# Kernel tuning notes

Measured on AMD Instinct MI355X. Metric: run time of the kernel, lower is better.

## Reference

```python
import jax, jax.numpy as jnp
import numpy as np

N_NODES = 65536
N_EDGES = 1048576
NODE_F = 32
EDGE_F = 8
HID = 64
OUT_F = 1
BATCH_SIZE = 64


def _glorot(key, shape):
    fan_in, fan_out = shape[0], shape[-1]
    s = jnp.sqrt(6.0 / (fan_in + fan_out))
    return jax.random.uniform(key, shape, jnp.float32, -s, s)


def setup_inputs() -> dict:
    key = jax.random.key(0)
    ks = jax.random.split(key, 20)
    inp = {
        "node_features": jax.random.normal(ks[0], (N_NODES, NODE_F), jnp.float32),
        "edge_features": jax.random.normal(ks[1], (N_EDGES, EDGE_F), jnp.float32),
        "Esrc": jax.random.randint(ks[2], (N_EDGES,), 0, N_NODES, jnp.int32),
        "Etgt": jax.random.randint(ks[3], (N_EDGES,), 0, N_NODES, jnp.int32),
        "batch": jnp.sort(jax.random.randint(ks[4], (N_NODES,), 0, BATCH_SIZE, jnp.int32)),
        # graph-conv weights
        "W_in": _glorot(ks[5], (NODE_F, HID)), "b_in": jnp.zeros((HID,), jnp.float32),
        "W_mid": _glorot(ks[6], (HID, HID)), "b_mid": jnp.zeros((HID,), jnp.float32),
        "W_out": _glorot(ks[7], (HID, OUT_F)), "b_out": jnp.zeros((OUT_F,), jnp.float32),
        # edge-encoder MLPs (Linear -> ReLU -> Linear)
        "ee_in_W1": _glorot(ks[8], (EDGE_F, HID)), "ee_in_b1": jnp.zeros((HID,), jnp.float32),
        "ee_in_W2": _glorot(ks[9], (HID, HID)), "ee_in_b2": jnp.zeros((HID,), jnp.float32),
        "ee_mid_W1": _glorot(ks[10], (EDGE_F, HID)), "ee_mid_b1": jnp.zeros((HID,), jnp.float32),
        "ee_mid_W2": _glorot(ks[11], (HID, HID)), "ee_mid_b2": jnp.zeros((HID,), jnp.float32),
        "ee_out_W1": _glorot(ks[12], (EDGE_F, OUT_F)), "ee_out_b1": jnp.zeros((OUT_F,), jnp.float32),
        "ee_out_W2": _glorot(ks[13], (OUT_F, OUT_F)), "ee_out_b2": jnp.zeros((OUT_F,), jnp.float32),
    }
    return inp


def _edge_mlp(ef, W1, b1, W2, b2):
    return jax.nn.relu(ef @ W1 + b1) @ W2 + b2  # [E, out]


def _egconv(x, W, b, Esrc, Etgt, edge_enc):
    support = x @ W                      # [N, out]
    msg = support[Esrc] * edge_enc       # [E, out] edge-gated messages
    agg = jax.ops.segment_sum(msg, Etgt, num_segments=N_NODES)  # [N, out]
    return agg + b


def reference(node_features, edge_features, Esrc, Etgt, batch,
              W_in, b_in, W_mid, b_mid, W_out, b_out,
              ee_in_W1, ee_in_b1, ee_in_W2, ee_in_b2,
              ee_mid_W1, ee_mid_b1, ee_mid_W2, ee_mid_b2,
              ee_out_W1, ee_out_b1, ee_out_W2, ee_out_b2):
    efin = _edge_mlp(edge_features, ee_in_W1, ee_in_b1, ee_in_W2, ee_in_b2)
    efmid = _edge_mlp(edge_features, ee_mid_W1, ee_mid_b1, ee_mid_W2, ee_mid_b2)
    efout = _edge_mlp(edge_features, ee_out_W1, ee_out_b1, ee_out_W2, ee_out_b2)

    x = jax.nn.relu(_egconv(node_features, W_in, b_in, Esrc, Etgt, efin))
    # dropout: identity in eval mode
    x = jax.nn.relu(_egconv(x, W_mid, b_mid, Esrc, Etgt, efmid))
    x = _egconv(x, W_out, b_out, Esrc, Etgt, efout)
    # graph-level sum pooling over batch ids
    out = jax.ops.segment_sum(x, batch, num_segments=BATCH_SIZE)  # [B, OUT_F]
    return out
```

## Files before the change

### kernel.cpp

```cpp
#include <hip/hip_runtime.h>

#define NN 65536
#define NE 1048576
#define NODE_F 32
#define EDGE_F 8
#define HID 64
#define NBATCH 64
#define NB 512
#define EPB (NE / NB)
#define NBIN 1024
#define CAP 2048

typedef __attribute__((ext_vector_type(8))) short s16x8;
typedef __attribute__((ext_vector_type(4))) float f32x4;

union FragU { s16x8 s; uint u[4]; };

__device__ inline uint pk2(float a, float b) {
    uint ua = __float_as_uint(a); ua += 0x7FFFu + ((ua >> 16) & 1u);
    uint ub = __float_as_uint(b); ub += 0x7FFFu + ((ub >> 16) & 1u);
    return (ua >> 16) | (ub & 0xFFFF0000u);
}

template<int K, bool RELUB>
__global__ __launch_bounds__(256) void node_linear(const float* __restrict__ x,
                                                   const float* __restrict__ pb,
                                                   const float* __restrict__ W,
                                                   float* __restrict__ out, int n_nodes) {
    const int lane = threadIdx.x & 63;
    const int wv = threadIdx.x >> 6;
    float wr[K];
#pragma unroll
    for (int k = 0; k < K; ++k) wr[k] = W[k * HID + lane];
    int wid = blockIdx.x * 4 + wv;
    const int nw = gridDim.x * 4;
    for (int n0 = wid; n0 < n_nodes; n0 += nw) {
        const int n = __builtin_amdgcn_readfirstlane(n0);
        const float* xr = x + (size_t)n * K;
        float acc = 0.f;
#pragma unroll
        for (int k = 0; k < K; ++k) {
            float xk = xr[k];
            if (RELUB) xk = fmaxf(xk + pb[k], 0.f);
            acc = fmaf(xk, wr[k], acc);
        }
        out[(size_t)n * HID + lane] = acc;
    }
}

__global__ __launch_bounds__(256) void p1_hist(const int* __restrict__ Etgt, int* __restrict__ bc,
                                               int* __restrict__ binTotal) {
    __shared__ int h[NBIN];
    const int blk = blockIdx.x;
    for (int t = threadIdx.x; t < NBIN; t += 256) h[t] = 0;
    __syncthreads();
    const int base = blk * EPB;
    for (int j = threadIdx.x; j < EPB; j += 256)
        atomicAdd(&h[((uint)Etgt[base + j]) >> 6], 1);
    __syncthreads();
    for (int t = threadIdx.x; t < NBIN; t += 256) {
        bc[blk * NBIN + t] = h[t];
        if (h[t]) atomicAdd(&binTotal[t], h[t]);
    }
}

__global__ __launch_bounds__(1024) void p2a_scan(const int* __restrict__ binTotal,
                                                 int* __restrict__ binStart) {
    __shared__ int part[NBIN];
    const int t = threadIdx.x;
    part[t] = binTotal[t];
    __syncthreads();
    for (int d = 1; d < NBIN; d <<= 1) {
        int v = part[t];
        int vo = (t >= d) ? part[t - d] : 0;
        __syncthreads();
        part[t] = v + vo;
        __syncthreads();
    }
    binStart[t + 1] = part[t];
    if (t == 0) binStart[0] = 0;
}

__global__ __launch_bounds__(256) void p2b_cursor(const int* __restrict__ bc,
                                                  const int* __restrict__ binStart,
                                                  int* __restrict__ cursor) {
    const int lane = threadIdx.x & 63;
    const int wv = threadIdx.x >> 6;
    const int bin = blockIdx.x * 4 + wv;
    int carry = binStart[bin];
    for (int c = 0; c < NB; c += 64) {
        const int blk = c + lane;
        const int v = bc[blk * NBIN + bin];
        int incl = v;
#pragma unroll
        for (int d = 1; d < 64; d <<= 1) {
            const int u = __shfl_up(incl, d, 64);
            if (lane >= d) incl += u;
        }
        cursor[blk * NBIN + bin] = carry + incl - v;
        carry += __shfl(incl, 63, 64);
    }
}

__global__ __launch_bounds__(256) void p3_scatter(
    const int* __restrict__ Etgt, const int* __restrict__ Esrc, const float* __restrict__ ef,
    const int* __restrict__ cursor, uint4* __restrict__ ef16_t, uint* __restrict__ stp_t)
{
    __shared__ int cur[NBIN];
    const int blk = blockIdx.x;
    for (int t = threadIdx.x; t < NBIN; t += 256) cur[t] = cursor[blk * NBIN + t];
    __syncthreads();
    const int base = blk * EPB;
    for (int j = threadIdx.x; j < EPB; j += 256) {
        const int i = base + j;
        const int tgt = Etgt[i];
        const int p = atomicAdd(&cur[(uint)tgt >> 6], 1);
        const float4 x = *(const float4*)(ef + (size_t)i * 8);
        const float4 y = *(const float4*)(ef + (size_t)i * 8 + 4);
        uint4 u;
        u.x = pk2(x.x, x.y); u.y = pk2(x.z, x.w);
        u.z = pk2(y.x, y.y); u.w = pk2(y.z, y.w);
        ef16_t[p] = u;
        stp_t[p] = (uint)Esrc[i] | ((uint)tgt << 16);
    }
}

__global__ __launch_bounds__(256) void p4_sort(
    const int* __restrict__ binStart, const uint* __restrict__ stp_t, const uint4* __restrict__ ef16_t,
    uint* __restrict__ stp, uint4* __restrict__ ef16)
{
    __shared__ uint s_stp[CAP];
    __shared__ int rk[CAP];
    __shared__ int cnt[64], off[64];
    const int b = blockIdx.x;
    const int beg = binStart[b], end = binStart[b + 1];
    const int n = end - beg;
    if (threadIdx.x < 64) cnt[threadIdx.x] = 0;
    __syncthreads();
    for (int j = threadIdx.x; j < n; j += 256) {
        const uint v = stp_t[beg + j];
        s_stp[j] = v;
        rk[j] = atomicAdd(&cnt[(v >> 16) & 63], 1);
    }
    __syncthreads();
    if (threadIdx.x == 0) {
        int run = 0;
#pragma unroll
        for (int k = 0; k < 64; ++k) { off[k] = run; run += cnt[k]; }
    }
    __syncthreads();
    for (int j = threadIdx.x; j < n; j += 256) {
        const uint v = s_stp[j];
        const int pos = beg + off[(v >> 16) & 63] + rk[j];
        stp[pos] = v;
        ef16[pos] = ef16_t[beg + j];
    }
}

#define ISSUE(BUF, BASE_)                                                        \
    _Pragma("unroll")                                                            \
    for (int jj = 0; jj < 16; ++jj) {                                            \
        const uint stj = (uint)__shfl((int)st_l, (BASE_) + jj, 64);              \
        sv##BUF[jj] = support[(size_t)(stj & 0xFFFFu) * HID + lane];             \
    }

#define PROC(BUF, BASE_)                                                         \
    _Pragma("unroll")                                                            \
    for (int jj = 0; jj < 16; ++jj) {                                            \
        const int j = (BASE_) + jj;                                              \
        const int tgt = (int)((uint)__shfl((int)st_l, j, 64) >> 16);             \
        const ushort eu = *(const ushort*)(lds + j * 128 + ((lane * 2) ^ ((j & 7) << 4))); \
        const float ev = __uint_as_float((uint)eu << 16) + b2l;                  \
        if (tgt != tprev) {                                                      \
            float* dst = agg + (size_t)tprev * HID + lane;                       \
            if (first) { atomicAdd(dst, acc); first = 0; }                       \
            else *dst = acc;                                                     \
            acc = 0.f; tprev = tgt;                                              \
        }                                                                        \
        acc = fmaf(sv##BUF[jj], ev, acc);                                        \
    }

__global__ __launch_bounds__(256, 4) void edge_layer_fused(
    const uint4* __restrict__ ef16, const uint* __restrict__ stp,
    const float* __restrict__ support,
    const float* __restrict__ W1, const float* __restrict__ b1,
    const float* __restrict__ W2, const float* __restrict__ b2,
    float* __restrict__ agg)
{
    __shared__ ushort lds_all[4][32 * 64];
    const int lane = threadIdx.x & 63;
    const int wv = threadIdx.x >> 6;
    char* lds = (char*)lds_all[wv];
    const int l15 = lane & 15, lhi = lane >> 4;
    const int swz = (l15 & 7) << 4;
    const float b2l = b2[lane];

    FragU a1[4];
#pragma unroll
    for (int mt = 0; mt < 4; ++mt) {
        a1[mt].u[0] = a1[mt].u[1] = a1[mt].u[2] = a1[mt].u[3] = 0;
        const int h = l15 + 16 * mt;
        if (lhi == 0) {
#pragma unroll
            for (int j = 0; j < 4; ++j)
                a1[mt].u[j] = pk2(W1[(2 * j) * HID + h], W1[(2 * j + 1) * HID + h]);
        } else if (lhi == 1) {
            a1[mt].u[0] = pk2(b1[h], 0.f);
        }
    }
    FragU a2[4][2];
#pragma unroll
    for (int mt = 0; mt < 4; ++mt)
#pragma unroll
        for (int kc = 0; kc < 2; ++kc) {
            const int o = l15 + 16 * mt;
            const int k0 = 32 * kc + 8 * lhi;
#pragma unroll
            for (int j = 0; j < 4; ++j)
                a2[mt][kc].u[j] = pk2(W2[(k0 + 2 * j) * HID + o], W2[(k0 + 2 * j + 1) * HID + o]);
        }

    for (int tile = blockIdx.x * 4 + wv; tile < NE / 32; tile += gridDim.x * 4) {
        const size_t ebase = (size_t)tile * 32;
        const uint st_l = stp[ebase + (lane & 31)];

#pragma unroll
        for (int nt = 0; nt < 2; ++nt) {
            FragU bf;
            bf.u[0] = bf.u[1] = bf.u[2] = bf.u[3] = 0;
            if (lhi == 0) {
                const uint4 u = ef16[ebase + nt * 16 + l15];
                bf.u[0] = u.x; bf.u[1] = u.y; bf.u[2] = u.z; bf.u[3] = u.w;
            } else if (lhi == 1) {
                bf.u[0] = 0x3F80u;
            }
            const int ebyte = (l15 + 16 * nt) * 128;
#pragma unroll
            for (int mt = 0; mt < 4; ++mt) {
                f32x4 c = {0.f, 0.f, 0.f, 0.f};
                c = __builtin_amdgcn_mfma_f32_16x16x32_bf16(a1[mt].s, bf.s, c, 0, 0, 0);
                uint2 w;
                w.x = pk2(fmaxf(c[0], 0.f), fmaxf(c[1], 0.f));
                w.y = pk2(fmaxf(c[2], 0.f), fmaxf(c[3], 0.f));
                const int hb = (16 * mt + 4 * lhi) * 2;
                *(uint2*)(lds + ebyte + (hb ^ swz)) = w;
            }
        }

        float svA[16], svB[16];
        int tprev = (int)((uint)__shfl((int)st_l, 0, 64) >> 16);
        int first = 1;
        float acc = 0.f;
        ISSUE(A, 0)
        ISSUE(B, 16)

#pragma unroll
        for (int nt = 0; nt < 2; ++nt) {
            const int ebyte = (l15 + 16 * nt) * 128;
            const s16x8 bh0 = *(const s16x8*)(lds + ebyte + ((16 * lhi + 0) ^ swz));
            const s16x8 bh1 = *(const s16x8*)(lds + ebyte + ((16 * lhi + 64) ^ swz));
#pragma unroll
            for (int mt = 0; mt < 4; ++mt) {
                f32x4 c = {0.f, 0.f, 0.f, 0.f};
                c = __builtin_amdgcn_mfma_f32_16x16x32_bf16(a2[mt][0].s, bh0, c, 0, 0, 0);
                c = __builtin_amdgcn_mfma_f32_16x16x32_bf16(a2[mt][1].s, bh1, c, 0, 0, 0);
                uint2 w;
                w.x = pk2(c[0], c[1]);
                w.y = pk2(c[2], c[3]);
                const int ob = (16 * mt + 4 * lhi) * 2;
                *(uint2*)(lds + ebyte + (ob ^ swz)) = w;
            }
        }

        PROC(A, 0)
        PROC(B, 16)
        atomicAdd(agg + (size_t)tprev * HID + lane, acc);
    }
}

__global__ __launch_bounds__(256) void node_dot(const float* __restrict__ x, const float* __restrict__ pb,
                                                const float* __restrict__ w,
                                                float* __restrict__ out, int n_nodes) {
    const int lane = threadIdx.x & 63;
    const int wv = threadIdx.x >> 6;
    const float wk = w[lane];
    const float pbv = pb[lane];
    int wid = blockIdx.x * 4 + wv;
    const int nw = gridDim.x * 4;
    for (int n = wid; n < n_nodes; n += nw) {
        float v = fmaxf(x[(size_t)n * HID + lane] + pbv, 0.f) * wk;
#pragma unroll
        for (int off = 32; off >= 1; off >>= 1) v += __shfl_xor(v, off, 64);
        if (lane == 0) out[n] = v;
    }
}

__global__ __launch_bounds__(256) void edge_out_fused(
    const float* __restrict__ ef, const int* __restrict__ Esrc, const int* __restrict__ Etgt,
    const float* __restrict__ sup3, const int* __restrict__ batch,
    const float* __restrict__ W1, const float* __restrict__ b1,
    const float* __restrict__ W2, const float* __restrict__ b2,
    float* __restrict__ out)
{
    __shared__ float accs[NBATCH];
    if (threadIdx.x < NBATCH) accs[threadIdx.x] = 0.f;
    __syncthreads();
    float w[8];
#pragma unroll
    for (int k = 0; k < 8; ++k) w[k] = W1[k];
    const float b1v = b1[0], w2 = W2[0], b2v = b2[0];
    int e = blockIdx.x * 256 + threadIdx.x;
    const int stride = gridDim.x * 256;
    for (; e < NE; e += stride) {
        const float4 a = *(const float4*)(ef + (size_t)e * 8);
        const float4 c = *(const float4*)(ef + (size_t)e * 8 + 4);
        float h = b1v;
        h = fmaf(a.x, w[0], h); h = fmaf(a.y, w[1], h);
        h = fmaf(a.z, w[2], h); h = fmaf(a.w, w[3], h);
        h = fmaf(c.x, w[4], h); h = fmaf(c.y, w[5], h);
        h = fmaf(c.z, w[6], h); h = fmaf(c.w, w[7], h);
        const float enc = fmaxf(h, 0.f) * w2 + b2v;
        const float msg = sup3[Esrc[e]] * enc;
        atomicAdd(&accs[batch[Etgt[e]]], msg);
    }
    __syncthreads();
    if (threadIdx.x < NBATCH) atomicAdd(&out[threadIdx.x], accs[threadIdx.x]);
}

__global__ __launch_bounds__(256) void pool_bias(const int* __restrict__ batch,
                                                 const float* __restrict__ b_out,
                                                 float* __restrict__ out) {
    __shared__ int cnt[NBATCH];
    if (threadIdx.x < NBATCH) cnt[threadIdx.x] = 0;
    __syncthreads();
    const int n = blockIdx.x * 256 + threadIdx.x;
    atomicAdd(&cnt[batch[n]], 1);
    __syncthreads();
    if (threadIdx.x < NBATCH && cnt[threadIdx.x])
        atomicAdd(&out[threadIdx.x], (float)cnt[threadIdx.x] * b_out[0]);
}

extern "C" void kernel_launch(void* const* d_in, const int* in_sizes, int n_in,
                              void* d_out, int out_size, void* d_ws, size_t ws_size,
                              hipStream_t stream) {
    const float* nf    = (const float*)d_in[0];
    const float* ef    = (const float*)d_in[1];
    const int*   Esrc  = (const int*)d_in[2];
    const int*   Etgt  = (const int*)d_in[3];
    const int*   batch = (const int*)d_in[4];
    const float* W_in  = (const float*)d_in[5];
    const float* b_in  = (const float*)d_in[6];
    const float* W_mid = (const float*)d_in[7];
    const float* b_mid = (const float*)d_in[8];
    const float* W_out = (const float*)d_in[9];
    const float* b_out = (const float*)d_in[10];
    const float* eiW1  = (const float*)d_in[11];
    const float* eib1  = (const float*)d_in[12];
    const float* eiW2  = (const float*)d_in[13];
    const float* eib2  = (const float*)d_in[14];
    const float* emW1  = (const float*)d_in[15];
    const float* emb1  = (const float*)d_in[16];
    const float* emW2  = (const float*)d_in[17];
    const float* emb2  = (const float*)d_in[18];
    const float* eoW1  = (const float*)d_in[19];
    const float* eob1  = (const float*)d_in[20];
    const float* eoW2  = (const float*)d_in[21];
    const float* eob2  = (const float*)d_in[22];

    float* bufA   = (float*)d_ws;
    float* bufB   = bufA + (size_t)NN * HID;
    float* sup3   = bufB + (size_t)NN * HID;
    uint4* ef16   = (uint4*)(sup3 + NN);
    uint*  stp    = (uint*)(ef16 + NE);
    uint4* ef16_t = (uint4*)(stp + NE);
    uint*  stp_t  = (uint*)(ef16_t + NE);
    int* bc       = (int*)(stp_t + NE);
    int* cursor   = bc + NB * NBIN;
    int* binStart = cursor + NB * NBIN;
    int* binTotal = binStart + NBIN + 1;

    hipMemsetAsync(d_out, 0, NBATCH * sizeof(float), stream);
    hipMemsetAsync(binTotal, 0, NBIN * sizeof(int), stream);

    p1_hist<<<NB, 256, 0, stream>>>(Etgt, bc, binTotal);
    p2a_scan<<<1, 1024, 0, stream>>>(binTotal, binStart);
    p2b_cursor<<<NBIN / 4, 256, 0, stream>>>(bc, binStart, cursor);
    p3_scatter<<<NB, 256, 0, stream>>>(Etgt, Esrc, ef, cursor, ef16_t, stp_t);
    p4_sort<<<NBIN, 256, 0, stream>>>(binStart, stp_t, ef16_t, stp, ef16);

    node_linear<NODE_F, false><<<1024, 256, 0, stream>>>(nf, nullptr, W_in, bufA, NN);
    hipMemsetAsync(bufB, 0, (size_t)NN * HID * sizeof(float), stream);
    edge_layer_fused<<<2048, 256, 0, stream>>>(ef16, stp, bufA, eiW1, eib1, eiW2, eib2, bufB);
    node_linear<HID, true><<<1024, 256, 0, stream>>>(bufB, b_in, W_mid, bufA, NN);
    hipMemsetAsync(bufB, 0, (size_t)NN * HID * sizeof(float), stream);
    edge_layer_fused<<<2048, 256, 0, stream>>>(ef16, stp, bufA, emW1, emb1, emW2, emb2, bufB);
    node_dot<<<256, 256, 0, stream>>>(bufB, b_mid, W_out, sup3, NN);
    edge_out_fused<<<1024, 256, 0, stream>>>(ef, Esrc, Etgt, sup3, batch,
                                             eoW1, eob1, eoW2, eob2, (float*)d_out);
    pool_bias<<<NN / 256, 256, 0, stream>>>(batch, b_out, (float*)d_out);
}
```

Before: 334.3 us.

## Replace per-target sort with per-bin LDS aggregation in edge layers

Drops the p4_sort pass that fully sorted edges by target within each 64-node bin. Each edge layer now launches one 512-thread block per bin, accumulates messages into a 64x64 LDS tile with LDS atomics, and writes the tile out directly. This also removes the two global memsets and the global atomics. The cost is one LDS atomic per edge per feature instead of run-length register accumulation, and the load per block depends on bin size (about 1024 edges each).

```diff
diff --git a/kernel.cpp b/kernel.cpp
--- a/kernel.cpp
+++ b/kernel.cpp
@@ -9,7 +9,6 @@
 #define NB 512
 #define EPB (NE / NB)
 #define NBIN 1024
-#define CAP 2048
 
 typedef __attribute__((ext_vector_type(8))) short s16x8;
 typedef __attribute__((ext_vector_type(4))) float f32x4;
@@ -104,7 +103,7 @@
 
 __global__ __launch_bounds__(256) void p3_scatter(
     const int* __restrict__ Etgt, const int* __restrict__ Esrc, const float* __restrict__ ef,
-    const int* __restrict__ cursor, uint4* __restrict__ ef16_t, uint* __restrict__ stp_t)
+    const int* __restrict__ cursor, uint4* __restrict__ ef16, uint* __restrict__ stp)
 {
     __shared__ int cur[NBIN];
     const int blk = blockIdx.x;
@@ -120,40 +119,8 @@
         uint4 u;
         u.x = pk2(x.x, x.y); u.y = pk2(x.z, x.w);
         u.z = pk2(y.x, y.y); u.w = pk2(y.z, y.w);
-        ef16_t[p] = u;
-        stp_t[p] = (uint)Esrc[i] | ((uint)tgt << 16);
-    }
-}
-
-__global__ __launch_bounds__(256) void p4_sort(
-    const int* __restrict__ binStart, const uint* __restrict__ stp_t, const uint4* __restrict__ ef16_t,
-    uint* __restrict__ stp, uint4* __restrict__ ef16)
-{
-    __shared__ uint s_stp[CAP];
-    __shared__ int rk[CAP];
-    __shared__ int cnt[64], off[64];
-    const int b = blockIdx.x;
-    const int beg = binStart[b], end = binStart[b + 1];
-    const int n = end - beg;
-    if (threadIdx.x < 64) cnt[threadIdx.x] = 0;
-    __syncthreads();
-    for (int j = threadIdx.x; j < n; j += 256) {
-        const uint v = stp_t[beg + j];
-        s_stp[j] = v;
-        rk[j] = atomicAdd(&cnt[(v >> 16) & 63], 1);
-    }
-    __syncthreads();
-    if (threadIdx.x == 0) {
-        int run = 0;
-#pragma unroll
-        for (int k = 0; k < 64; ++k) { off[k] = run; run += cnt[k]; }
-    }
-    __syncthreads();
-    for (int j = threadIdx.x; j < n; j += 256) {
-        const uint v = s_stp[j];
-        const int pos = beg + off[(v >> 16) & 63] + rk[j];
-        stp[pos] = v;
-        ef16[pos] = ef16_t[beg + j];
+        ef16[p] = u;
+        stp[p] = (uint)Esrc[i] | ((uint)tgt << 16);
     }
 }
 
@@ -168,32 +135,32 @@
     _Pragma("unroll")                                                            \
     for (int jj = 0; jj < 16; ++jj) {                                            \
         const int j = (BASE_) + jj;                                              \
-        const int tgt = (int)((uint)__shfl((int)st_l, j, 64) >> 16);             \
-        const ushort eu = *(const ushort*)(lds + j * 128 + ((lane * 2) ^ ((j & 7) << 4))); \
-        const float ev = __uint_as_float((uint)eu << 16) + b2l;                  \
-        if (tgt != tprev) {                                                      \
-            float* dst = agg + (size_t)tprev * HID + lane;                       \
-            if (first) { atomicAdd(dst, acc); first = 0; }                       \
-            else *dst = acc;                                                     \
-            acc = 0.f; tprev = tgt;                                              \
+        if (j < nvalid) {                                                        \
+            const uint stj = (uint)__shfl((int)st_l, j, 64);                     \
+            const int t6 = (int)((stj >> 16) & 63u);                             \
+            const ushort eu = *(const ushort*)(lds + j * 128 + ((lane * 2) ^ ((j & 7) << 4))); \
+            const float ev = __uint_as_float((uint)eu << 16) + b2l;              \
+            atomicAdd(&aggl[t6][lane], sv##BUF[jj] * ev);                        \
         }                                                                        \
-        acc = fmaf(sv##BUF[jj], ev, acc);                                        \
-    }
-
-__global__ __launch_bounds__(256, 4) void edge_layer_fused(
+    }
+
+__global__ __launch_bounds__(512, 4) void edge_layer_bin(
     const uint4* __restrict__ ef16, const uint* __restrict__ stp,
-    const float* __restrict__ support,
+    const int* __restrict__ binStart, const float* __restrict__ support,
     const float* __restrict__ W1, const float* __restrict__ b1,
     const float* __restrict__ W2, const float* __restrict__ b2,
     float* __restrict__ agg)
 {
-    __shared__ ushort lds_all[4][32 * 64];
+    __shared__ float aggl[64][64];
+    __shared__ ushort enc_all[8][32 * 64];
     const int lane = threadIdx.x & 63;
     const int wv = threadIdx.x >> 6;
-    char* lds = (char*)lds_all[wv];
+    char* lds = (char*)enc_all[wv];
     const int l15 = lane & 15, lhi = lane >> 4;
     const int swz = (l15 & 7) << 4;
     const float b2l = b2[lane];
+
+    for (int t = threadIdx.x; t < 64 * 64; t += 512) ((float*)aggl)[t] = 0.f;
 
     FragU a1[4];
 #pragma unroll
@@ -220,17 +187,25 @@
                 a2[mt][kc].u[j] = pk2(W2[(k0 + 2 * j) * HID + o], W2[(k0 + 2 * j + 1) * HID + o]);
         }
 
-    for (int tile = blockIdx.x * 4 + wv; tile < NE / 32; tile += gridDim.x * 4) {
-        const size_t ebase = (size_t)tile * 32;
-        const uint st_l = stp[ebase + (lane & 31)];
+    const int bin = blockIdx.x;
+    const int beg = binStart[bin];
+    const int end = binStart[bin + 1];
+    __syncthreads();
+
+    for (int ebase = beg + wv * 32; ebase < end; ebase += 8 * 32) {
+        const int nvalid = min(32, end - ebase);
+        uint st_l = 0;
+        if ((lane & 31) < nvalid) st_l = stp[ebase + (lane & 31)];
 
 #pragma unroll
         for (int nt = 0; nt < 2; ++nt) {
             FragU bf;
             bf.u[0] = bf.u[1] = bf.u[2] = bf.u[3] = 0;
             if (lhi == 0) {
-                const uint4 u = ef16[ebase + nt * 16 + l15];
-                bf.u[0] = u.x; bf.u[1] = u.y; bf.u[2] = u.z; bf.u[3] = u.w;
+                if (nt * 16 + l15 < nvalid) {
+                    const uint4 u = ef16[ebase + nt * 16 + l15];
+                    bf.u[0] = u.x; bf.u[1] = u.y; bf.u[2] = u.z; bf.u[3] = u.w;
+                }
             } else if (lhi == 1) {
                 bf.u[0] = 0x3F80u;
             }
@@ -248,9 +223,6 @@
         }
 
         float svA[16], svB[16];
-        int tprev = (int)((uint)__shfl((int)st_l, 0, 64) >> 16);
-        int first = 1;
-        float acc = 0.f;
         ISSUE(A, 0)
         ISSUE(B, 16)
 
@@ -274,8 +246,12 @@
 
         PROC(A, 0)
         PROC(B, 16)
-        atomicAdd(agg + (size_t)tprev * HID + lane, acc);
-    }
+    }
+
+    __syncthreads();
+    float4* ag4 = (float4*)aggl;
+    float4* out4 = (float4*)(agg + (size_t)bin * 64 * HID);
+    for (int t = threadIdx.x; t < 64 * HID / 4; t += 512) out4[t] = ag4[t];
 }
 
 __global__ __launch_bounds__(256) void node_dot(const float* __restrict__ x, const float* __restrict__ pb,
@@ -372,9 +348,7 @@
     float* sup3   = bufB + (size_t)NN * HID;
     uint4* ef16   = (uint4*)(sup3 + NN);
     uint*  stp    = (uint*)(ef16 + NE);
-    uint4* ef16_t = (uint4*)(stp + NE);
-    uint*  stp_t  = (uint*)(ef16_t + NE);
-    int* bc       = (int*)(stp_t + NE);
+    int* bc       = (int*)(stp + NE);
     int* cursor   = bc + NB * NBIN;
     int* binStart = cursor + NB * NBIN;
     int* binTotal = binStart + NBIN + 1;
@@ -385,15 +359,14 @@
     p1_hist<<<NB, 256, 0, stream>>>(Etgt, bc, binTotal);
     p2a_scan<<<1, 1024, 0, stream>>>(binTotal, binStart);
     p2b_cursor<<<NBIN / 4, 256, 0, stream>>>(bc, binStart, cursor);
-    p3_scatter<<<NB, 256, 0, stream>>>(Etgt, Esrc, ef, cursor, ef16_t, stp_t);
-    p4_sort<<<NBIN, 256, 0, stream>>>(binStart, stp_t, ef16_t, stp, ef16);
+    p3_scatter<<<NB, 256, 0, stream>>>(Etgt, Esrc, ef, cursor, ef16, stp);
 
     node_linear<NODE_F, false><<<1024, 256, 0, stream>>>(nf, nullptr, W_in, bufA, NN);
-    hipMemsetAsync(bufB, 0, (size_t)NN * HID * sizeof(float), stream);
-    edge_layer_fused<<<2048, 256, 0, stream>>>(ef16, stp, bufA, eiW1, eib1, eiW2, eib2, bufB);
+    edge_layer_bin<<<NBIN, 512, 0, stream>>>(ef16, stp, binStart, bufA,
+                                             eiW1, eib1, eiW2, eib2, bufB);
     node_linear<HID, true><<<1024, 256, 0, stream>>>(bufB, b_in, W_mid, bufA, NN);
-    hipMemsetAsync(bufB, 0, (size_t)NN * HID * sizeof(float), stream);
-    edge_layer_fused<<<2048, 256, 0, stream>>>(ef16, stp, bufA, emW1, emb1, emW2, emb2, bufB);
+    edge_layer_bin<<<NBIN, 512, 0, stream>>>(ef16, stp, binStart, bufA,
+                                             emW1, emb1, emW2, emb2, bufB);
     node_dot<<<256, 256, 0, stream>>>(bufB, b_mid, W_out, sup3, NN);
     edge_out_fused<<<1024, 256, 0, stream>>>(ef, Esrc, Etgt, sup3, batch,
                                              eoW1, eob1, eoW2, eob2, (float*)d_out);
```

After: 956.6 us. 186% more time.

## Precompute final edge encoding in scatter and pool sorted edges per wave

Applied to the files above, without the earlier changes.

The scalar output-layer edge encoding is now computed during the scatter pass and carried through the sort as an extra float per edge. The last layer then reads the target-sorted edges, accumulates runs of equal batch id per lane, and reduces across the wave when all lanes share a batch. This replaces the old kernel that reread the full fp32 edge features and did one shared-memory atomic per edge. Separately, wave-uniform shuffles in the edge layer become readlane intrinsics. The cost is an extra 4-byte write and copy per edge in the sort passes.

```diff
diff --git a/kernel.cpp b/kernel.cpp
--- a/kernel.cpp
+++ b/kernel.cpp
@@ -104,11 +104,18 @@
 
 __global__ __launch_bounds__(256) void p3_scatter(
     const int* __restrict__ Etgt, const int* __restrict__ Esrc, const float* __restrict__ ef,
-    const int* __restrict__ cursor, uint4* __restrict__ ef16_t, uint* __restrict__ stp_t)
+    const int* __restrict__ cursor,
+    const float* __restrict__ oW1, const float* __restrict__ ob1,
+    const float* __restrict__ oW2, const float* __restrict__ ob2,
+    uint4* __restrict__ ef16_t, uint* __restrict__ stp_t, float* __restrict__ enc3_t)
 {
     __shared__ int cur[NBIN];
     const int blk = blockIdx.x;
     for (int t = threadIdx.x; t < NBIN; t += 256) cur[t] = cursor[blk * NBIN + t];
+    float w[8];
+#pragma unroll
+    for (int k = 0; k < 8; ++k) w[k] = oW1[k];
+    const float b1v = ob1[0], w2 = oW2[0], b2v = ob2[0];
     __syncthreads();
     const int base = blk * EPB;
     for (int j = threadIdx.x; j < EPB; j += 256) {
@@ -122,12 +129,19 @@
         u.z = pk2(y.x, y.y); u.w = pk2(y.z, y.w);
         ef16_t[p] = u;
         stp_t[p] = (uint)Esrc[i] | ((uint)tgt << 16);
+        float h = b1v;
+        h = fmaf(x.x, w[0], h); h = fmaf(x.y, w[1], h);
+        h = fmaf(x.z, w[2], h); h = fmaf(x.w, w[3], h);
+        h = fmaf(y.x, w[4], h); h = fmaf(y.y, w[5], h);
+        h = fmaf(y.z, w[6], h); h = fmaf(y.w, w[7], h);
+        enc3_t[p] = fmaxf(h, 0.f) * w2 + b2v;
     }
 }
 
 __global__ __launch_bounds__(256) void p4_sort(
-    const int* __restrict__ binStart, const uint* __restrict__ stp_t, const uint4* __restrict__ ef16_t,
-    uint* __restrict__ stp, uint4* __restrict__ ef16)
+    const int* __restrict__ binStart, const uint* __restrict__ stp_t,
+    const uint4* __restrict__ ef16_t, const float* __restrict__ enc3_t,
+    uint* __restrict__ stp, uint4* __restrict__ ef16, float* __restrict__ enc3)
 {
     __shared__ uint s_stp[CAP];
     __shared__ int rk[CAP];
@@ -154,13 +168,14 @@
         const int pos = beg + off[(v >> 16) & 63] + rk[j];
         stp[pos] = v;
         ef16[pos] = ef16_t[beg + j];
+        enc3[pos] = enc3_t[beg + j];
     }
 }
 
 #define ISSUE(BUF, BASE_)                                                        \
     _Pragma("unroll")                                                            \
     for (int jj = 0; jj < 16; ++jj) {                                            \
-        const uint stj = (uint)__shfl((int)st_l, (BASE_) + jj, 64);              \
+        const uint stj = (uint)__builtin_amdgcn_readlane((int)st_l, (BASE_) + jj); \
         sv##BUF[jj] = support[(size_t)(stj & 0xFFFFu) * HID + lane];             \
     }
 
@@ -168,7 +183,7 @@
     _Pragma("unroll")                                                            \
     for (int jj = 0; jj < 16; ++jj) {                                            \
         const int j = (BASE_) + jj;                                              \
-        const int tgt = (int)((uint)__shfl((int)st_l, j, 64) >> 16);             \
+        const int tgt = (int)((uint)__builtin_amdgcn_readlane((int)st_l, j) >> 16); \
         const ushort eu = *(const ushort*)(lds + j * 128 + ((lane * 2) ^ ((j & 7) << 4))); \
         const float ev = __uint_as_float((uint)eu << 16) + b2l;                  \
         if (tgt != tprev) {                                                      \
@@ -248,7 +263,7 @@
         }
 
         float svA[16], svB[16];
-        int tprev = (int)((uint)__shfl((int)st_l, 0, 64) >> 16);
+        int tprev = (int)((uint)__builtin_amdgcn_readlane((int)st_l, 0) >> 16);
         int first = 1;
         float acc = 0.f;
         ISSUE(A, 0)
@@ -295,36 +310,38 @@
     }
 }
 
-__global__ __launch_bounds__(256) void edge_out_fused(
-    const float* __restrict__ ef, const int* __restrict__ Esrc, const int* __restrict__ Etgt,
+__global__ __launch_bounds__(256) void edge_out_seg(
+    const uint* __restrict__ stp, const float* __restrict__ enc3,
     const float* __restrict__ sup3, const int* __restrict__ batch,
-    const float* __restrict__ W1, const float* __restrict__ b1,
-    const float* __restrict__ W2, const float* __restrict__ b2,
     float* __restrict__ out)
 {
-    __shared__ float accs[NBATCH];
-    if (threadIdx.x < NBATCH) accs[threadIdx.x] = 0.f;
-    __syncthreads();
-    float w[8];
-#pragma unroll
-    for (int k = 0; k < 8; ++k) w[k] = W1[k];
-    const float b1v = b1[0], w2 = W2[0], b2v = b2[0];
-    int e = blockIdx.x * 256 + threadIdx.x;
-    const int stride = gridDim.x * 256;
-    for (; e < NE; e += stride) {
-        const float4 a = *(const float4*)(ef + (size_t)e * 8);
-        const float4 c = *(const float4*)(ef + (size_t)e * 8 + 4);
-        float h = b1v;
-        h = fmaf(a.x, w[0], h); h = fmaf(a.y, w[1], h);
-        h = fmaf(a.z, w[2], h); h = fmaf(a.w, w[3], h);
-        h = fmaf(c.x, w[4], h); h = fmaf(c.y, w[5], h);
-        h = fmaf(c.z, w[6], h); h = fmaf(c.w, w[7], h);
-        const float enc = fmaxf(h, 0.f) * w2 + b2v;
-        const float msg = sup3[Esrc[e]] * enc;
-        atomicAdd(&accs[batch[Etgt[e]]], msg);
-    }
-    __syncthreads();
-    if (threadIdx.x < NBATCH) atomicAdd(&out[threadIdx.x], accs[threadIdx.x]);
+    const int lane = threadIdx.x & 63;
+    const int wv = threadIdx.x >> 6;
+    const size_t base = ((size_t)blockIdx.x * 4 + wv) * 128;
+    float acc = 0.f;
+    int bcur = -1;
+#pragma unroll
+    for (int c = 0; c < 2; ++c) {
+        const size_t i = base + c * 64 + lane;
+        const uint st = stp[i];
+        const float m = sup3[st & 0xFFFFu] * enc3[i];
+        const int b = batch[st >> 16];
+        if (b != bcur) {
+            if (bcur >= 0) atomicAdd(&out[bcur], acc);
+            bcur = b;
+            acc = m;
+        } else {
+            acc += m;
+        }
+    }
+    const int b0 = __builtin_amdgcn_readfirstlane(bcur);
+    if (__all(bcur == b0)) {
+#pragma unroll
+        for (int off = 32; off >= 1; off >>= 1) acc += __shfl_xor(acc, off, 64);
+        if (lane == 0) atomicAdd(&out[b0], acc);
+    } else {
+        atomicAdd(&out[bcur], acc);
+    }
 }
 
 __global__ __launch_bounds__(256) void pool_bias(const int* __restrict__ batch,
@@ -372,9 +389,11 @@
     float* sup3   = bufB + (size_t)NN * HID;
     uint4* ef16   = (uint4*)(sup3 + NN);
     uint*  stp    = (uint*)(ef16 + NE);
-    uint4* ef16_t = (uint4*)(stp + NE);
+    float* enc3   = (float*)(stp + NE);
+    uint4* ef16_t = (uint4*)(enc3 + NE);
     uint*  stp_t  = (uint*)(ef16_t + NE);
-    int* bc       = (int*)(stp_t + NE);
+    float* enc3_t = (float*)(stp_t + NE);
+    int* bc       = (int*)(enc3_t + NE);
     int* cursor   = bc + NB * NBIN;
     int* binStart = cursor + NB * NBIN;
     int* binTotal = binStart + NBIN + 1;
@@ -385,8 +404,9 @@
     p1_hist<<<NB, 256, 0, stream>>>(Etgt, bc, binTotal);
     p2a_scan<<<1, 1024, 0, stream>>>(binTotal, binStart);
     p2b_cursor<<<NBIN / 4, 256, 0, stream>>>(bc, binStart, cursor);
-    p3_scatter<<<NB, 256, 0, stream>>>(Etgt, Esrc, ef, cursor, ef16_t, stp_t);
-    p4_sort<<<NBIN, 256, 0, stream>>>(binStart, stp_t, ef16_t, stp, ef16);
+    p3_scatter<<<NB, 256, 0, stream>>>(Etgt, Esrc, ef, cursor,
+                                       eoW1, eob1, eoW2, eob2, ef16_t, stp_t, enc3_t);
+    p4_sort<<<NBIN, 256, 0, stream>>>(binStart, stp_t, ef16_t, enc3_t, stp, ef16, enc3);
 
     node_linear<NODE_F, false><<<1024, 256, 0, stream>>>(nf, nullptr, W_in, bufA, NN);
     hipMemsetAsync(bufB, 0, (size_t)NN * HID * sizeof(float), stream);
@@ -395,7 +415,6 @@
     hipMemsetAsync(bufB, 0, (size_t)NN * HID * sizeof(float), stream);
     edge_layer_fused<<<2048, 256, 0, stream>>>(ef16, stp, bufA, emW1, emb1, emW2, emb2, bufB);
     node_dot<<<256, 256, 0, stream>>>(bufB, b_mid, W_out, sup3, NN);
-    edge_out_fused<<<1024, 256, 0, stream>>>(ef, Esrc, Etgt, sup3, batch,
-                                             eoW1, eob1, eoW2, eob2, (float*)d_out);
+    edge_out_seg<<<NE / 512, 256, 0, stream>>>(stp, enc3, sup3, batch, (float*)d_out);
     pool_bias<<<NN / 256, 256, 0, stream>>>(batch, b_out, (float*)d_out);
 }
```

Result: slower. 398.4 us (+19.2%).
